# Kernel optimization log

Measured on AMD Instinct MI355X. Metric: run time of the kernel, lower is better.

## Reference

```python
import jax, jax.numpy as jnp
import numpy as np

B, T, V, F = 32, 128, 128, 64
K_ORDER = 3
N_FILT = 64

def setup_inputs() -> dict:
    key = jax.random.key(0)
    k1, k2, k3 = jax.random.split(key, 3)
    x = jax.random.normal(k1, (B, T, V, F), dtype=jnp.float32)
    W = jax.random.uniform(k2, (B, V, V), dtype=jnp.float32)  # learned adjacency, nonneg
    # keras 'uniform' initializer default range [-0.05, 0.05]
    Theta = jax.random.uniform(k3, (K_ORDER, F, N_FILT), dtype=jnp.float32, minval=-0.05, maxval=0.05)
    return {"x": x, "W": W, "Theta": Theta}

def reference(x, W, Theta):
    # x: (B,T,V,F), W: (B,V,V), Theta: (k,F,O)
    k = Theta.shape[0]
    v = x.shape[2]
    eye = jnp.eye(v, dtype=x.dtype)
    deg = jnp.sum(W, axis=1)                      # (B,V) -- sum over axis=1 as in K.sum(W, axis=1)
    D = eye[None, :, :] * deg[:, :, None]         # matrix_diag(deg)
    L = D - W
    L_t = L - eye[None, :, :]                     # 2*L/lambda_max - I with lambda_max=2
    chebs = [jnp.broadcast_to(eye[None, :, :], W.shape), L_t]
    for i in range(2, k):
        # NOTE: elementwise multiply, faithful to the original tf code (tf `*`)
        chebs.append(2.0 * L_t * chebs[-1] - chebs[-2])
    Tk = jnp.stack(chebs, axis=0)                 # (k,B,V,V)
    # out[b,t,u,o] = sum_{k,v,f} Tk[k,b,v,u] * x[b,t,v,f] * Theta[k,f,o]
    # (T_k transposed matmul graph_signal, then dot with theta_k, summed over k and t-batched)
    out = jnp.einsum('kbvu,btvf,kfo->btuo', Tk, x, Theta)
    return jax.nn.relu(out)
```

## Files before the change

kernel.cpp:

```cpp
#include <hip/hip_runtime.h>

typedef __attribute__((ext_vector_type(8))) short bf16x8;
typedef __attribute__((ext_vector_type(4))) float f32x4;

namespace {

constexpr int B = 32, T = 128, V = 128, F = 64, O = 64;
constexpr int TPB = 16;

constexpr size_t WS_THT_OFF = (size_t)B * 64 * 64 * 8 * 2;
constexpr size_t WS_LDG_OFF = WS_THT_OFF + 1536 * 8 * 2;

__device__ inline unsigned short f2bf(float f) {
    unsigned u = __builtin_bit_cast(unsigned, f);
    u += 0x7FFFu + ((u >> 16) & 1u);
    return (unsigned short)(u >> 16);
}

__global__ __launch_bounds__(256) void prep(const float* __restrict__ W,
                                            const float* __restrict__ Theta,
                                            unsigned short* __restrict__ acat_f,
                                            unsigned short* __restrict__ tht_f,
                                            float* __restrict__ ldg) {
    const int tid = threadIdx.x;
    if (blockIdx.x == B) {
        for (int i = 0; i < 6; ++i) {
            int fi = tid + i * 256;
            int ks = fi / 768, rem = fi % 768;
            int nf = rem >> 6, lane = rem & 63;
            int n = nf * 16 + (lane & 15);
            int f0 = ks * 32 + (lane >> 4) * 8;
            unsigned short vals[8];
#pragma unroll
            for (int j = 0; j < 8; ++j) {
                int f = f0 + j;
                float v;
                if (n < 64)       v = Theta[f * 64 + n] - Theta[2 * 4096 + f * 64 + n];
                else if (n < 128) v = Theta[4096 + f * 64 + (n - 64)];
                else              v = Theta[2 * 4096 + f * 64 + (n - 128)];
                vals[j] = f2bf(v);
            }
            *(bf16x8*)(tht_f + (size_t)fi * 8) = *(bf16x8*)vals;
        }
        return;
    }
    const int b = blockIdx.x;
    const float* Wb = W + (size_t)b * V * V;
    __shared__ float Wl[V][V + 1];
    for (int i = 0; i < V * V / 256; ++i) {
        int idx = tid + i * 256;
        Wl[idx >> 7][idx & 127] = Wb[idx];
    }
    __syncthreads();
    if (tid < V) {
        float s = 0.f;
        for (int i = 0; i < V; ++i) s += Wl[i][tid];
        ldg[b * V + tid] = s - 1.0f - Wl[tid][tid];
    }
    unsigned short* ab_f = acat_f + (size_t)b * 32768;
    for (int i = 0; i < 16; ++i) {
        int fi = tid + i * 256;
        int ks = fi >> 9, rem = fi & 511;
        int r2 = rem >> 6, lane = rem & 63;
        int u = r2 * 16 + (lane & 15);
        int kv0 = ks * 32 + (lane >> 4) * 8;
        unsigned short vals[8];
#pragma unroll
        for (int j = 0; j < 8; ++j) {
            int kv = kv0 + j, v = kv & 127;
            float wv = Wl[v][u];
            float val = (v == u) ? 0.f : ((kv < 128) ? -wv : 2.f * wv * wv);
            vals[j] = f2bf(val);
        }
        *(bf16x8*)(ab_f + (size_t)fi * 8) = *(bf16x8*)vals;
    }
}

__global__ __launch_bounds__(512, 2) void graph_conv_main(
    const float* __restrict__ x, const unsigned short* __restrict__ acat_f,
    const unsigned short* __restrict__ tht_f, const float* __restrict__ ldg,
    float* __restrict__ out) {
    const int t0 = blockIdx.x * TPB, b = blockIdx.y;
    const int tid = threadIdx.x;
    const int lane = tid & 63, w = tid >> 6;
    const int lr = lane & 15, lg = lane >> 4;

    __shared__ __align__(16) unsigned short tht_s[12288];
    __shared__ __align__(16) float xbuf[2][V * F];
    __shared__ __align__(16) unsigned short zc1[8192];
    __shared__ __align__(16) unsigned short zc2[8192];

    const float* xb = x + ((size_t)(b * T + t0)) * (V * F);

    bf16x8 af_r[8];
#pragma unroll
    for (int ks = 0; ks < 8; ++ks)
        af_r[ks] = *(const bf16x8*)(acat_f + (((size_t)b * 64 + ks * 8 + w) * 64 + lane) * 8);
    const f32x4 ldv = *(const f32x4*)(ldg + b * V + 16 * w + lg * 4);
    const f32x4 ld2v = 2.0f * ldv * ldv;
    asm volatile("s_waitcnt vmcnt(0)" ::: "memory");
    __builtin_amdgcn_sched_barrier(0);

    auto stage_x = [&](int tt, int buf) {
        const char* src = (const char*)(xb + (size_t)tt * (V * F));
        char* lbase = (char*)&xbuf[buf][0] + w * 4096;
#pragma unroll
        for (int j = 0; j < 4; ++j) {
            int a = j * 1024 + lane * 16;
            int rloc = a >> 8;
            int slot = (a >> 5) & 7;
            int within = a & 31;
            int row = 16 * w + rloc;
            const char* g = src + row * 256 + ((slot ^ (row & 7)) << 5) + within;
            __builtin_amdgcn_global_load_lds(
                (const __attribute__((address_space(1))) void*)g,
                (__attribute__((address_space(3))) void*)(lbase + j * 1024), 16, 0, 0);
        }
    };

#pragma unroll
    for (int i = 0; i < 3; ++i) {
        int c = tid + i * 512;
        __builtin_amdgcn_global_load_lds(
            (const __attribute__((address_space(1))) void*)(tht_f + c * 8),
            (__attribute__((address_space(3))) void*)(tht_s + c * 8), 16, 0, 0);
    }
    stage_x(0, 0);
    asm volatile("s_waitcnt vmcnt(0)" ::: "memory");
    __builtin_amdgcn_sched_barrier(0);
    __builtin_amdgcn_s_barrier();
    __builtin_amdgcn_sched_barrier(0);

    int cur = 0;
    for (int tt = 0; tt < TPB; ++tt) {
        if (tt + 1 < TPB) stage_x(tt + 1, cur ^ 1);
        asm volatile("s_waitcnt vmcnt(4)" ::: "memory");
        __builtin_amdgcn_sched_barrier(0);

        bf16x8 xa[2];
        {
            const int row = 16 * w + lr;
            const char* rbp = (const char*)&xbuf[cur][0] + row * 256;
            const int rs = row & 7;
#pragma unroll
            for (int ks = 0; ks < 2; ++ks) {
                const char* pa = rbp + (((ks * 4 + lg) ^ rs) << 5);
                f32x4 a0 = *(const f32x4*)pa;
                f32x4 a1 = *(const f32x4*)(pa + 16);
                uint4 u;
                u.x = f2bf(a0[0]) | ((unsigned)f2bf(a0[1]) << 16);
                u.y = f2bf(a0[2]) | ((unsigned)f2bf(a0[3]) << 16);
                u.z = f2bf(a1[0]) | ((unsigned)f2bf(a1[1]) << 16);
                u.w = f2bf(a1[2]) | ((unsigned)f2bf(a1[3]) << 16);
                xa[ks] = __builtin_bit_cast(bf16x8, u);
            }
        }

        f32x4 acc[4], z[4];
#pragma unroll
        for (int of = 0; of < 4; ++of) {
            acc[of] = (f32x4){0.f, 0.f, 0.f, 0.f};
            z[of] = (f32x4){0.f, 0.f, 0.f, 0.f};
        }

#pragma unroll
        for (int ks = 0; ks < 2; ++ks)
#pragma unroll
            for (int nf = 0; nf < 8; ++nf) {
                bf16x8 tb = *(const bf16x8*)(tht_s + ((ks * 12 + nf) * 64 + lane) * 8);
                if (nf < 4) acc[nf] = __builtin_amdgcn_mfma_f32_16x16x32_bf16(xa[ks], tb, acc[nf], 0, 0, 0);
                else        z[nf - 4] = __builtin_amdgcn_mfma_f32_16x16x32_bf16(xa[ks], tb, z[nf - 4], 0, 0, 0);
            }

        {
            const int vcol = 16 * w + lg * 4;
#pragma unroll
            for (int of = 0; of < 4; ++of) {
                acc[of] += ldv * z[of];
                const int rowz = of * 16 + lr;
                f32x4 zv = z[of];
                uint2 q;
                q.x = f2bf(zv[0]) | ((unsigned)f2bf(zv[1]) << 16);
                q.y = f2bf(zv[2]) | ((unsigned)f2bf(zv[3]) << 16);
                *(uint2*)((char*)zc1 + rowz * 256 + ((vcol * 2) ^ ((rowz & 7) << 4))) = q;
                z[of] = (f32x4){0.f, 0.f, 0.f, 0.f};
            }
        }

#pragma unroll
        for (int ks = 0; ks < 2; ++ks)
#pragma unroll
            for (int nf = 0; nf < 4; ++nf) {
                bf16x8 tb = *(const bf16x8*)(tht_s + ((ks * 12 + 8 + nf) * 64 + lane) * 8);
                z[nf] = __builtin_amdgcn_mfma_f32_16x16x32_bf16(xa[ks], tb, z[nf], 0, 0, 0);
            }

        {
            const int vcol = 16 * w + lg * 4;
#pragma unroll
            for (int of = 0; of < 4; ++of) {
                acc[of] += ld2v * z[of];
                const int rowz = of * 16 + lr;
                f32x4 zv = z[of];
                uint2 q;
                q.x = f2bf(zv[0]) | ((unsigned)f2bf(zv[1]) << 16);
                q.y = f2bf(zv[2]) | ((unsigned)f2bf(zv[3]) << 16);
                *(uint2*)((char*)zc2 + rowz * 256 + ((vcol * 2) ^ ((rowz & 7) << 4))) = q;
            }
        }

        asm volatile("s_waitcnt lgkmcnt(0)" ::: "memory");
        __builtin_amdgcn_sched_barrier(0);
        __builtin_amdgcn_s_barrier();
        __builtin_amdgcn_sched_barrier(0);

#pragma unroll
        for (int ks = 0; ks < 8; ++ks) {
            const char* zsrc = (ks < 4) ? (const char*)zc1 : (const char*)zc2;
            const int kcol = (ks & 3) * 64 + lg * 16;
#pragma unroll
            for (int of = 0; of < 4; ++of) {
                const int rowz = of * 16 + lr;
                bf16x8 zb = *(const bf16x8*)(zsrc + rowz * 256 + (kcol ^ ((rowz & 7) << 4)));
                acc[of] = __builtin_amdgcn_mfma_f32_16x16x32_bf16(af_r[ks], zb, acc[of], 0, 0, 0);
            }
        }

        float* obt = out + ((size_t)(b * T + t0 + tt)) * (V * O);
#pragma unroll
        for (int of = 0; of < 4; ++of)
#pragma unroll
            for (int j = 0; j < 4; ++j) {
                const int u = 16 * w + lg * 4 + j;
                const int o = of * 16 + lr;
                const float r = acc[of][j];
                obt[u * 64 + o] = r > 0.f ? r : 0.f;
            }

        asm volatile("s_waitcnt lgkmcnt(0)" ::: "memory");
        __builtin_amdgcn_sched_barrier(0);
        __builtin_amdgcn_s_barrier();
        __builtin_amdgcn_sched_barrier(0);
        cur ^= 1;
    }
}

}

extern "C" void kernel_launch(void* const* d_in, const int* in_sizes, int n_in,
                              void* d_out, int out_size, void* d_ws, size_t ws_size,
                              hipStream_t stream) {
    const float* x = (const float*)d_in[0];
    const float* W = (const float*)d_in[1];
    const float* Theta = (const float*)d_in[2];
    float* outp = (float*)d_out;

    unsigned short* acat_f = (unsigned short*)d_ws;
    unsigned short* tht_f = (unsigned short*)((char*)d_ws + WS_THT_OFF);
    float* ldg = (float*)((char*)d_ws + WS_LDG_OFF);

    prep<<<B + 1, 256, 0, stream>>>(W, Theta, acat_f, tht_f, ldg);
    graph_conv_main<<<dim3(T / TPB, B), 512, 0, stream>>>(x, acat_f, tht_f, ldg, outp);
}
```

Baseline: 87.94 us.

## Retile waves to 32x32 output blocks and keep Theta in registers

Each wave now covers a 32-vertex by 32-output block (vertex quarter and output half) instead of 16 vertices by all outputs. This halves LDS reads of the z operand per MFMA and lets the Theta fragments each wave needs sit in registers, which removes the tht_s shared buffer. The x staging swizzle is changed to 16-byte granularity with a new XOR pattern, and the end-of-iteration barrier is moved to the top of the loop. Launch bounds drop to one block per SIMD pair, so register pressure rises and occupancy may fall.

```diff
diff --git a/kernel.cpp b/kernel.cpp
--- a/kernel.cpp
+++ b/kernel.cpp
@@ -76,138 +76,142 @@
     }
 }
 
-__global__ __launch_bounds__(512, 2) void graph_conv_main(
+__global__ __launch_bounds__(512, 1) void graph_conv_main(
     const float* __restrict__ x, const unsigned short* __restrict__ acat_f,
     const unsigned short* __restrict__ tht_f, const float* __restrict__ ldg,
     float* __restrict__ out) {
     const int t0 = blockIdx.x * TPB, b = blockIdx.y;
     const int tid = threadIdx.x;
     const int lane = tid & 63, w = tid >> 6;
+    const int uq = w & 3;
+    const int oh = w >> 2;
     const int lr = lane & 15, lg = lane >> 4;
 
-    __shared__ __align__(16) unsigned short tht_s[12288];
     __shared__ __align__(16) float xbuf[2][V * F];
     __shared__ __align__(16) unsigned short zc1[8192];
     __shared__ __align__(16) unsigned short zc2[8192];
 
     const float* xb = x + ((size_t)(b * T + t0)) * (V * F);
 
-    bf16x8 af_r[8];
+    bf16x8 af_r[2][8];
 #pragma unroll
     for (int ks = 0; ks < 8; ++ks)
-        af_r[ks] = *(const bf16x8*)(acat_f + (((size_t)b * 64 + ks * 8 + w) * 64 + lane) * 8);
-    const f32x4 ldv = *(const f32x4*)(ldg + b * V + 16 * w + lg * 4);
-    const f32x4 ld2v = 2.0f * ldv * ldv;
-    asm volatile("s_waitcnt vmcnt(0)" ::: "memory");
-    __builtin_amdgcn_sched_barrier(0);
+#pragma unroll
+        for (int uf = 0; uf < 2; ++uf)
+            af_r[uf][ks] = *(const bf16x8*)(acat_f +
+                (((size_t)b * 64 + ks * 8 + 2 * uq + uf) * 64 + lane) * 8);
+
+    bf16x8 th_r[3][2][2];
+#pragma unroll
+    for (int m = 0; m < 3; ++m)
+#pragma unroll
+        for (int i = 0; i < 2; ++i)
+#pragma unroll
+            for (int kf = 0; kf < 2; ++kf) {
+                int nf = m * 4 + 2 * oh + i;
+                th_r[m][i][kf] = *(const bf16x8*)(tht_f + ((size_t)(kf * 12 + nf) * 64 + lane) * 8);
+            }
+
+    f32x4 ldv[2], ld2v[2];
+#pragma unroll
+    for (int uf = 0; uf < 2; ++uf) {
+        ldv[uf] = *(const f32x4*)(ldg + b * V + 32 * uq + 16 * uf + lg * 4);
+        ld2v[uf] = 2.0f * ldv[uf] * ldv[uf];
+    }
 
     auto stage_x = [&](int tt, int buf) {
         const char* src = (const char*)(xb + (size_t)tt * (V * F));
-        char* lbase = (char*)&xbuf[buf][0] + w * 4096;
+        char* dst = (char*)&xbuf[buf][0] + w * 4096;
 #pragma unroll
         for (int j = 0; j < 4; ++j) {
-            int a = j * 1024 + lane * 16;
-            int rloc = a >> 8;
-            int slot = (a >> 5) & 7;
-            int within = a & 31;
+            int n = j * 64 + lane;
+            int rloc = n >> 4, slot = n & 15;
+            int e = ((rloc & 3) << 1) | ((rloc >> 3) & 1);
             int row = 16 * w + rloc;
-            const char* g = src + row * 256 + ((slot ^ (row & 7)) << 5) + within;
+            const char* g = src + row * 256 + ((slot ^ e) << 4);
             __builtin_amdgcn_global_load_lds(
                 (const __attribute__((address_space(1))) void*)g,
-                (__attribute__((address_space(3))) void*)(lbase + j * 1024), 16, 0, 0);
+                (__attribute__((address_space(3))) void*)(dst + n * 16), 16, 0, 0);
         }
     };
 
-#pragma unroll
-    for (int i = 0; i < 3; ++i) {
-        int c = tid + i * 512;
-        __builtin_amdgcn_global_load_lds(
-            (const __attribute__((address_space(1))) void*)(tht_f + c * 8),
-            (__attribute__((address_space(3))) void*)(tht_s + c * 8), 16, 0, 0);
-    }
     stage_x(0, 0);
     asm volatile("s_waitcnt vmcnt(0)" ::: "memory");
     __builtin_amdgcn_sched_barrier(0);
     __builtin_amdgcn_s_barrier();
     __builtin_amdgcn_sched_barrier(0);
 
-    int cur = 0;
+    const int eL = ((lr & 3) << 1) | ((lr >> 3) & 1);
+
     for (int tt = 0; tt < TPB; ++tt) {
-        if (tt + 1 < TPB) stage_x(tt + 1, cur ^ 1);
-        asm volatile("s_waitcnt vmcnt(4)" ::: "memory");
-        __builtin_amdgcn_sched_barrier(0);
-
-        bf16x8 xa[2];
-        {
-            const int row = 16 * w + lr;
-            const char* rbp = (const char*)&xbuf[cur][0] + row * 256;
-            const int rs = row & 7;
-#pragma unroll
-            for (int ks = 0; ks < 2; ++ks) {
-                const char* pa = rbp + (((ks * 4 + lg) ^ rs) << 5);
-                f32x4 a0 = *(const f32x4*)pa;
-                f32x4 a1 = *(const f32x4*)(pa + 16);
+        const int cur = tt & 1;
+
+        if (tt + 1 < TPB) {
+            stage_x(tt + 1, cur ^ 1);
+            asm volatile("s_waitcnt vmcnt(4)" ::: "memory");
+        } else {
+            asm volatile("s_waitcnt vmcnt(0)" ::: "memory");
+        }
+        __builtin_amdgcn_sched_barrier(0);
+        __builtin_amdgcn_s_barrier();
+        __builtin_amdgcn_sched_barrier(0);
+
+        bf16x8 xa[2][2];
+        const char* xc = (const char*)&xbuf[cur][0];
+#pragma unroll
+        for (int rv = 0; rv < 2; ++rv) {
+            const char* rp = xc + (32 * uq + 16 * rv + lr) * 256;
+#pragma unroll
+            for (int kf = 0; kf < 2; ++kf) {
+                const int s0 = kf * 8 + lg * 2;
+                f32x4 a0 = *(const f32x4*)(rp + ((s0 ^ eL) << 4));
+                f32x4 a1 = *(const f32x4*)(rp + (((s0 + 1) ^ eL) << 4));
                 uint4 u;
                 u.x = f2bf(a0[0]) | ((unsigned)f2bf(a0[1]) << 16);
                 u.y = f2bf(a0[2]) | ((unsigned)f2bf(a0[3]) << 16);
                 u.z = f2bf(a1[0]) | ((unsigned)f2bf(a1[1]) << 16);
                 u.w = f2bf(a1[2]) | ((unsigned)f2bf(a1[3]) << 16);
-                xa[ks] = __builtin_bit_cast(bf16x8, u);
-            }
-        }
-
-        f32x4 acc[4], z[4];
-#pragma unroll
-        for (int of = 0; of < 4; ++of) {
-            acc[of] = (f32x4){0.f, 0.f, 0.f, 0.f};
-            z[of] = (f32x4){0.f, 0.f, 0.f, 0.f};
-        }
-
-#pragma unroll
-        for (int ks = 0; ks < 2; ++ks)
-#pragma unroll
-            for (int nf = 0; nf < 8; ++nf) {
-                bf16x8 tb = *(const bf16x8*)(tht_s + ((ks * 12 + nf) * 64 + lane) * 8);
-                if (nf < 4) acc[nf] = __builtin_amdgcn_mfma_f32_16x16x32_bf16(xa[ks], tb, acc[nf], 0, 0, 0);
-                else        z[nf - 4] = __builtin_amdgcn_mfma_f32_16x16x32_bf16(xa[ks], tb, z[nf - 4], 0, 0, 0);
-            }
-
-        {
-            const int vcol = 16 * w + lg * 4;
-#pragma unroll
-            for (int of = 0; of < 4; ++of) {
-                acc[of] += ldv * z[of];
-                const int rowz = of * 16 + lr;
-                f32x4 zv = z[of];
-                uint2 q;
-                q.x = f2bf(zv[0]) | ((unsigned)f2bf(zv[1]) << 16);
-                q.y = f2bf(zv[2]) | ((unsigned)f2bf(zv[3]) << 16);
-                *(uint2*)((char*)zc1 + rowz * 256 + ((vcol * 2) ^ ((rowz & 7) << 4))) = q;
-                z[of] = (f32x4){0.f, 0.f, 0.f, 0.f};
-            }
-        }
-
-#pragma unroll
-        for (int ks = 0; ks < 2; ++ks)
-#pragma unroll
-            for (int nf = 0; nf < 4; ++nf) {
-                bf16x8 tb = *(const bf16x8*)(tht_s + ((ks * 12 + 8 + nf) * 64 + lane) * 8);
-                z[nf] = __builtin_amdgcn_mfma_f32_16x16x32_bf16(xa[ks], tb, z[nf], 0, 0, 0);
-            }
-
-        {
-            const int vcol = 16 * w + lg * 4;
-#pragma unroll
-            for (int of = 0; of < 4; ++of) {
-                acc[of] += ld2v * z[of];
-                const int rowz = of * 16 + lr;
-                f32x4 zv = z[of];
-                uint2 q;
-                q.x = f2bf(zv[0]) | ((unsigned)f2bf(zv[1]) << 16);
-                q.y = f2bf(zv[2]) | ((unsigned)f2bf(zv[3]) << 16);
-                *(uint2*)((char*)zc2 + rowz * 256 + ((vcol * 2) ^ ((rowz & 7) << 4))) = q;
-            }
-        }
+                xa[rv][kf] = __builtin_bit_cast(bf16x8, u);
+            }
+        }
+
+        f32x4 acc[2][2], z1[2][2], z2[2][2];
+#pragma unroll
+        for (int a = 0; a < 2; ++a)
+#pragma unroll
+            for (int o = 0; o < 2; ++o) {
+                acc[a][o] = (f32x4){0.f, 0.f, 0.f, 0.f};
+                z1[a][o] = (f32x4){0.f, 0.f, 0.f, 0.f};
+                z2[a][o] = (f32x4){0.f, 0.f, 0.f, 0.f};
+            }
+#pragma unroll
+        for (int kf = 0; kf < 2; ++kf)
+#pragma unroll
+            for (int rv = 0; rv < 2; ++rv)
+#pragma unroll
+                for (int i = 0; i < 2; ++i) {
+                    acc[rv][i] = __builtin_amdgcn_mfma_f32_16x16x32_bf16(xa[rv][kf], th_r[0][i][kf], acc[rv][i], 0, 0, 0);
+                    z1[rv][i] = __builtin_amdgcn_mfma_f32_16x16x32_bf16(xa[rv][kf], th_r[1][i][kf], z1[rv][i], 0, 0, 0);
+                    z2[rv][i] = __builtin_amdgcn_mfma_f32_16x16x32_bf16(xa[rv][kf], th_r[2][i][kf], z2[rv][i], 0, 0, 0);
+                }
+
+#pragma unroll
+        for (int uf = 0; uf < 2; ++uf)
+#pragma unroll
+            for (int of = 0; of < 2; ++of) {
+                acc[uf][of] += ldv[uf] * z1[uf][of] + ld2v[uf] * z2[uf][of];
+                const int ro = 32 * oh + of * 16 + lr;
+                const int slot = 4 * uq + 2 * uf + (lg >> 1);
+                const int byte = ro * 256 + (((slot ^ eL)) << 4) + (lg & 1) * 8;
+                f32x4 v1 = z1[uf][of], v2 = z2[uf][of];
+                uint2 q1, q2;
+                q1.x = f2bf(v1[0]) | ((unsigned)f2bf(v1[1]) << 16);
+                q1.y = f2bf(v1[2]) | ((unsigned)f2bf(v1[3]) << 16);
+                q2.x = f2bf(v2[0]) | ((unsigned)f2bf(v2[1]) << 16);
+                q2.y = f2bf(v2[2]) | ((unsigned)f2bf(v2[3]) << 16);
+                *(uint2*)((char*)zc1 + byte) = q1;
+                *(uint2*)((char*)zc2 + byte) = q2;
+            }
 
         asm volatile("s_waitcnt lgkmcnt(0)" ::: "memory");
         __builtin_amdgcn_sched_barrier(0);
@@ -215,33 +219,34 @@
         __builtin_amdgcn_sched_barrier(0);
 
 #pragma unroll
-        for (int ks = 0; ks < 8; ++ks) {
-            const char* zsrc = (ks < 4) ? (const char*)zc1 : (const char*)zc2;
-            const int kcol = (ks & 3) * 64 + lg * 16;
-#pragma unroll
-            for (int of = 0; of < 4; ++of) {
-                const int rowz = of * 16 + lr;
-                bf16x8 zb = *(const bf16x8*)(zsrc + rowz * 256 + (kcol ^ ((rowz & 7) << 4)));
-                acc[of] = __builtin_amdgcn_mfma_f32_16x16x32_bf16(af_r[ks], zb, acc[of], 0, 0, 0);
-            }
+        for (int kk = 0; kk < 8; ++kk) {
+            const char* zsrc = (kk < 4) ? (const char*)zc1 : (const char*)zc2;
+            bf16x8 zb[2];
+#pragma unroll
+            for (int of = 0; of < 2; ++of) {
+                const int ro = 32 * oh + of * 16 + lr;
+                const int slot = (kk & 3) * 4 + lg;
+                zb[of] = *(const bf16x8*)(zsrc + ro * 256 + ((slot ^ eL) << 4));
+            }
+#pragma unroll
+            for (int uf = 0; uf < 2; ++uf)
+#pragma unroll
+                for (int of = 0; of < 2; ++of)
+                    acc[uf][of] = __builtin_amdgcn_mfma_f32_16x16x32_bf16(af_r[uf][kk], zb[of], acc[uf][of], 0, 0, 0);
         }
 
         float* obt = out + ((size_t)(b * T + t0 + tt)) * (V * O);
 #pragma unroll
-        for (int of = 0; of < 4; ++of)
-#pragma unroll
-            for (int j = 0; j < 4; ++j) {
-                const int u = 16 * w + lg * 4 + j;
-                const int o = of * 16 + lr;
-                const float r = acc[of][j];
-                obt[u * 64 + o] = r > 0.f ? r : 0.f;
-            }
-
-        asm volatile("s_waitcnt lgkmcnt(0)" ::: "memory");
-        __builtin_amdgcn_sched_barrier(0);
-        __builtin_amdgcn_s_barrier();
-        __builtin_amdgcn_sched_barrier(0);
-        cur ^= 1;
+        for (int uf = 0; uf < 2; ++uf)
+#pragma unroll
+            for (int of = 0; of < 2; ++of)
+#pragma unroll
+                for (int j = 0; j < 4; ++j) {
+                    const int u = 32 * uq + 16 * uf + lg * 4 + j;
+                    const int o = 32 * oh + 16 * of + lr;
+                    const float r = acc[uf][of][j];
+                    obt[u * 64 + o] = r > 0.f ? r : 0.f;
+                }
     }
 }
 
```

After: 92.34 us. 1.05x slower.
